# Kernel optimization log

Hardware: AMD Instinct MI355X
Metric: run time of the kernel (lower is better)

## Reference

```python
import jax, jax.numpy as jnp
import numpy as np

N = 50000      # nodes
E = 640000     # edges
DIN = 128      # input feature dim
DOUT = 128     # env net output dim
DACT = 2       # action net output dim (keep/drop logits)
REL = 100      # relation embedding dim (hard-coded in get_net)
T = 2          # num edge types
TAU = 0.5      # gumbel temperature (CoGNN temp)


def _lin(k, i, o):
    return jax.random.normal(k, (o, i), jnp.float32) * np.float32(1.0 / np.sqrt(i))


def _hgn_params(key, din, dout):
    ks = jax.random.split(key, 5)
    return {"W_w": _lin(ks[0], din, dout), "W_b": jnp.zeros((dout,), jnp.float32),
            "Wr_w": _lin(ks[1], REL, dout), "Wr_b": jnp.zeros((dout,), jnp.float32),
            "a_w": _lin(ks[2], 3 * dout, 1), "a_b": jnp.zeros((1,), jnp.float32),
            "Wres_w": _lin(ks[3], din, dout), "Wres_b": jnp.zeros((dout,), jnp.float32),
            "rel_emb": jax.random.normal(ks[4], (T, REL), jnp.float32)}


def setup_inputs():
    key = jax.random.key(0)
    ks = jax.random.split(key, 8)
    inp = {"x": jax.random.normal(ks[0], (N, DIN), jnp.float32),
           "edge_index": jax.random.randint(ks[1], (2, E), 0, N, jnp.int32),
           "edge_type": jax.random.randint(ks[2], (E,), 0, T, jnp.int32)}
    u_in = jax.random.uniform(ks[3], (N, DACT), jnp.float32, 1e-6, 1.0 - 1e-6)
    u_out = jax.random.uniform(ks[4], (N, DACT), jnp.float32, 1e-6, 1.0 - 1e-6)
    inp["g_in"] = -jnp.log(-jnp.log(u_in))    # Gumbel(0,1) noise
    inp["g_out"] = -jnp.log(-jnp.log(u_out))
    for name, k, dout in (("inA", ks[5], DACT), ("outA", ks[6], DACT), ("env", ks[7], DOUT)):
        for pk, pv in _hgn_params(k, DIN, dout).items():
            inp[name + "_" + pk] = pv
    return inp


def _simple_hgn(x, src, dst, etype, W_w, W_b, Wr_w, Wr_b, a_w, a_b, Wres_w, Wres_b, rel_emb, mask=None):
    # out = scatter_add_dst( alpha_e * W x_src ) + W_res x   (SimpleHGN, add aggr)
    n = x.shape[0]
    dout = W_w.shape[0]
    h = x @ W_w.T + W_b                       # [N, dout] = W(x)
    r = rel_emb @ Wr_w.T + Wr_b               # [T, dout] = W_r(rel_emb)
    # a(cat(W(x_i), W(x_j), W_r(rel))) decomposed into three per-node/per-type dot products
    a1, a2, a3 = a_w[0, :dout], a_w[0, dout:2 * dout], a_w[0, 2 * dout:]
    s_dst = h @ a1                            # [N]
    s_src = h @ a2                            # [N]
    s_rel = r @ a3                            # [T]
    logits = jax.nn.leaky_relu(s_dst[dst] + s_src[src] + s_rel[etype] + a_b[0], 0.2)  # [E]
    if mask is not None:
        logits = jnp.where(mask, logits, -1e9)
    m = jax.ops.segment_max(logits, dst, num_segments=n)
    e = jnp.exp(logits - m[dst])
    if mask is not None:
        e = jnp.where(mask, e, 0.0)
    denom = jax.ops.segment_sum(e, dst, num_segments=n)
    alpha = e / jnp.maximum(denom[dst], 1e-16)   # edge softmax over incoming edges of each target
    aggr = jax.ops.segment_sum(h[src] * alpha[:, None], dst, num_segments=n)
    return aggr + x @ Wres_w.T + Wres_b


def _gumbel_hard(logits, g):
    y = jax.nn.softmax((logits + g) / TAU, axis=-1)
    y_hard = jax.nn.one_hot(jnp.argmax(y, axis=-1), y.shape[-1], dtype=y.dtype)
    return y_hard + y - jax.lax.stop_gradient(y)   # straight-through (hard=True)


def reference(x, edge_index, edge_type, g_in, g_out,
              inA_W_w, inA_W_b, inA_Wr_w, inA_Wr_b, inA_a_w, inA_a_b, inA_Wres_w, inA_Wres_b, inA_rel_emb,
              outA_W_w, outA_W_b, outA_Wr_w, outA_Wr_b, outA_a_w, outA_a_b, outA_Wres_w, outA_Wres_b, outA_rel_emb,
              env_W_w, env_W_b, env_Wr_w, env_Wr_b, env_a_w, env_a_b, env_Wres_w, env_Wres_b, env_rel_emb):
    src, dst = edge_index[0], edge_index[1]
    in_logits = _simple_hgn(x, src, dst, edge_type, inA_W_w, inA_W_b, inA_Wr_w, inA_Wr_b,
                            inA_a_w, inA_a_b, inA_Wres_w, inA_Wres_b, inA_rel_emb)
    out_logits = _simple_hgn(x, src, dst, edge_type, outA_W_w, outA_W_b, outA_Wr_w, outA_Wr_b,
                             outA_a_w, outA_a_b, outA_Wres_w, outA_Wres_b, outA_rel_emb)
    in_p = _gumbel_hard(in_logits, g_in)
    out_p = _gumbel_hard(out_logits, g_out)
    edge_weight = in_p[:, 0][dst] * out_p[:, 0][src]   # keep_in[v] * keep_out[u]
    mask = edge_weight > 0                              # hard edge filtering, non-differentiable as in torch
    return _simple_hgn(x, src, dst, edge_type, env_W_w, env_W_b, env_Wr_w, env_Wr_b,
                       env_a_w, env_a_b, env_Wres_w, env_Wres_b, env_rel_emb, mask=mask)
```

## Files before the change

### kernel.cpp

```cpp
#include <hip/hip_runtime.h>
#include <hip/hip_bf16.h>
#include <hip/hip_fp16.h>
#include <cstddef>

#define N_NODES 50000
#define N_EDGES 640000
#define DEG_CAP 48

__device__ __forceinline__ float lrelu(float z) { return z >= 0.f ? z : 0.2f * z; }

__device__ __forceinline__ unsigned short f2bf(float f) {
    unsigned u = __builtin_bit_cast(unsigned, f);
    u += 0x7FFFu + ((u >> 16) & 1u);
    return (unsigned short)(u >> 16);
}
__device__ __forceinline__ float bf2f(unsigned short h) {
    unsigned u = ((unsigned)h) << 16;
    return __builtin_bit_cast(float, u);
}

typedef __attribute__((ext_vector_type(8))) short short8;
typedef __attribute__((ext_vector_type(4))) float floatx4;

__global__ __launch_bounds__(256) void k_setup(
    const float* __restrict__ x,
    const float* __restrict__ rel_in, const float* __restrict__ Wr_in,
    const float* __restrict__ Wrb_in,
    const float* __restrict__ rel_out, const float* __restrict__ Wr_out,
    const float* __restrict__ Wrb_out,
    const float* __restrict__ rel_env, const float* __restrict__ Wr_env,
    const float* __restrict__ Wrb_env,
    const float* __restrict__ Wi, const float* __restrict__ Wib,
    const float* __restrict__ WiR, const float* __restrict__ WiRb,
    const float* __restrict__ ai,
    const float* __restrict__ Wo, const float* __restrict__ Wob,
    const float* __restrict__ WoR, const float* __restrict__ WoRb,
    const float* __restrict__ ao,
    const float* __restrict__ eW, const float* __restrict__ eWb,
    const float* __restrict__ eWR, const float* __restrict__ ea,
    float* __restrict__ srel,
    unsigned short* __restrict__ wh, unsigned short* __restrict__ wl,
    float4* __restrict__ dstT, float4* __restrict__ srcPack,
    float4* __restrict__ res_pack, int* __restrict__ cursor)
{
    int b = blockIdx.x;
    int tid = threadIdx.x;

    if (b == 0) {
        __shared__ float red[256];
        __shared__ float rs[8];
        {
            int tt = tid >> 7, j = tid & 127;
            float acc = 0.f;
            for (int k = 0; k < 100; ++k) acc += rel_env[tt * 100 + k] * Wr_env[j * 100 + k];
            acc += Wrb_env[j];
            red[tid] = acc * ea[256 + j];
        }
        if (tid < 8) {
            int net = tid >> 2, tt = (tid >> 1) & 1, j = tid & 1;
            const float* re = net ? rel_out : rel_in;
            const float* wr = net ? Wr_out : Wr_in;
            const float* wb = net ? Wrb_out : Wrb_in;
            float acc = 0.f;
            for (int k = 0; k < 100; ++k) acc += re[tt * 100 + k] * wr[j * 100 + k];
            rs[tid] = acc + wb[j];
        }
        __syncthreads();
        if (tid < 2) {
            float s = 0.f;
            for (int j = 0; j < 128; ++j) s += red[tid * 128 + j];
            srel[4 + tid] = s;
        } else if (tid == 2) {
            srel[0] = rs[0] * ai[4] + rs[1] * ai[5];
            srel[1] = rs[2] * ai[4] + rs[3] * ai[5];
        } else if (tid == 3) {
            srel[2] = rs[4] * ao[4] + rs[5] * ao[5];
            srel[3] = rs[6] * ao[4] + rs[7] * ao[5];
        }
        return;
    }
    if (b < 129) {
        int i = (b - 1) * 256 + tid;
        float v = (i < 16384) ? eW[i] : eWR[i - 16384];
        unsigned short h = f2bf(v);
        wh[i] = h;
        wl[i] = f2bf(v - bf2f(h));
        return;
    }

    int n = (b - 129) * 256 + tid;
    if (n < N_NODES) cursor[n] = 0;

    __shared__ float sw[10][128];
    __shared__ float vb[2];
    {
        int row = tid >> 5, c4 = tid & 31;
        const float* src;
        switch (row) {
            case 0: src = Wi;        break;
            case 1: src = Wi + 128;  break;
            case 2: src = WiR;       break;
            case 3: src = WiR + 128; break;
            case 4: src = Wo;        break;
            case 5: src = Wo + 128;  break;
            case 6: src = WoR;       break;
            default: src = WoR + 128; break;
        }
        float4 v = ((const float4*)src)[c4];
        sw[row][c4 * 4 + 0] = v.x; sw[row][c4 * 4 + 1] = v.y;
        sw[row][c4 * 4 + 2] = v.z; sw[row][c4 * 4 + 3] = v.w;
    }
    {
        int half = tid >> 7, k = tid & 127;
        const float* av = ea + half * 128;
        float s = 0.f;
        for (int j = 0; j < 128; ++j) s += eW[j * 128 + k] * av[j];
        sw[8 + half][k] = s;
    }
    if (tid < 2) {
        const float* av2 = ea + tid * 128;
        float sb = 0.f;
        for (int j = 0; j < 128; ++j) sb += eWb[j] * av2[j];
        vb[tid] = sb;
    }
    __syncthreads();
    if (n >= N_NODES) return;
    const float4* xr = (const float4*)(x + (size_t)n * 128);
    float a0 = 0, a1 = 0, a2 = 0, a3 = 0, a4 = 0, a5 = 0, a6 = 0, a7 = 0;
    float a8 = 0, a9 = 0;
#pragma unroll 8
    for (int k4 = 0; k4 < 32; ++k4) {
        float4 v = xr[k4];
        int k = k4 * 4;
        a0 += v.x * sw[0][k] + v.y * sw[0][k + 1] + v.z * sw[0][k + 2] + v.w * sw[0][k + 3];
        a1 += v.x * sw[1][k] + v.y * sw[1][k + 1] + v.z * sw[1][k + 2] + v.w * sw[1][k + 3];
        a2 += v.x * sw[2][k] + v.y * sw[2][k + 1] + v.z * sw[2][k + 2] + v.w * sw[2][k + 3];
        a3 += v.x * sw[3][k] + v.y * sw[3][k + 1] + v.z * sw[3][k + 2] + v.w * sw[3][k + 3];
        a4 += v.x * sw[4][k] + v.y * sw[4][k + 1] + v.z * sw[4][k + 2] + v.w * sw[4][k + 3];
        a5 += v.x * sw[5][k] + v.y * sw[5][k + 1] + v.z * sw[5][k + 2] + v.w * sw[5][k + 3];
        a6 += v.x * sw[6][k] + v.y * sw[6][k + 1] + v.z * sw[6][k + 2] + v.w * sw[6][k + 3];
        a7 += v.x * sw[7][k] + v.y * sw[7][k + 1] + v.z * sw[7][k + 2] + v.w * sw[7][k + 3];
        a8 += v.x * sw[8][k] + v.y * sw[8][k + 1] + v.z * sw[8][k + 2] + v.w * sw[8][k + 3];
        a9 += v.x * sw[9][k] + v.y * sw[9][k + 1] + v.z * sw[9][k + 2] + v.w * sw[9][k + 3];
    }
    float hi0 = a0 + Wib[0], hi1 = a1 + Wib[1];
    float ri0 = a2 + WiRb[0], ri1 = a3 + WiRb[1];
    float ho0 = a4 + Wob[0], ho1 = a5 + Wob[1];
    float ro0 = a6 + WoRb[0], ro1 = a7 + WoRb[1];
    float sdi = hi0 * ai[0] + hi1 * ai[1];
    float ssi = hi0 * ai[2] + hi1 * ai[3];
    float sdo = ho0 * ao[0] + ho1 * ao[1];
    float sso = ho0 * ao[2] + ho1 * ao[3];
    dstT[n]           = make_float4(sdi, sdo, a8 + vb[0], 0.f);
    srcPack[2 * n]     = make_float4(ssi, sso, a9 + vb[1], 0.f);
    srcPack[2 * n + 1] = make_float4(hi0, hi1, ho0, ho1);
    res_pack[n]       = make_float4(ri0, ri1, ro0, ro1);
}

__global__ __launch_bounds__(256, 2) void k_mid(
    const float* __restrict__ x,
    const unsigned short* __restrict__ wh, const unsigned short* __restrict__ wl,
    const float* __restrict__ Wb, const float* __restrict__ WRb,
    __half* __restrict__ h_env, float* __restrict__ dout,
    const int* __restrict__ ei, const int* __restrict__ et,
    const float4* __restrict__ dstT, const float4* __restrict__ srcPack,
    const float* __restrict__ srel, const float* __restrict__ ab_env,
    int* __restrict__ cursor, unsigned long long* __restrict__ recs)
{
    int b = blockIdx.x;
    int tid = threadIdx.x;

    if (b >= 512) {
        int base = (b - 512) * 1024 + tid;
        float s4 = srel[4], s5 = srel[5];
        float abe = ab_env[0];
        int src[4], dst[4], t[4];
#pragma unroll
        for (int k = 0; k < 4; ++k) {
            int e = base + k * 256;
            src[k] = ei[e];
            dst[k] = ei[N_EDGES + e];
            t[k]   = et[e];
        }
        float4 dT[4], sT[4];
#pragma unroll
        for (int k = 0; k < 4; ++k) {
            dT[k] = dstT[dst[k]];
            sT[k] = srcPack[2 * src[k]];
        }
#pragma unroll
        for (int k = 0; k < 4; ++k) {
            float le = lrelu(dT[k].z + sT[k].z + (t[k] ? s5 : s4) + abe);
            int pos = atomicAdd(&cursor[dst[k]], 1);
            if (pos < DEG_CAP) {
                unsigned lo = (unsigned)(src[k] | (t[k] << 20));
                unsigned hi = (unsigned)__float_as_int(__expf(le));
                recs[dst[k] * DEG_CAP + pos] = ((unsigned long long)hi << 32) | lo;
            }
        }
        return;
    }

    int lane = tid & 63;
    int wv = tid >> 6;
    int l15 = lane & 15;
    int quad = lane >> 4;
    int jbase = wv * 64;

    short8 bh[4][4], bl[4][4];
    float bias[4];
#pragma unroll
    for (int jtl = 0; jtl < 4; ++jtl) {
        int j = jbase + jtl * 16 + l15;
        bias[jtl] = (j < 128) ? Wb[j] : WRb[j - 128];
#pragma unroll
        for (int ks = 0; ks < 4; ++ks) {
            size_t o = (size_t)j * 128 + ks * 32 + quad * 8;
            bh[jtl][ks] = *(const short8*)(wh + o);
            bl[jtl][ks] = *(const short8*)(wl + o);
        }
    }

    for (int t = b; t < 3125; t += 512) {
        int node = t * 16 + l15;
        const float4* ap = (const float4*)(x + (size_t)node * 128 + quad * 8);
        float4 f[8];
#pragma unroll
        for (int ks = 0; ks < 4; ++ks) {
            f[2 * ks]     = ap[ks * 8];
            f[2 * ks + 1] = ap[ks * 8 + 1];
        }
        short8 ah[4], al[4];
#pragma unroll
        for (int ks = 0; ks < 4; ++ks) {
            float av[8] = {f[2 * ks].x, f[2 * ks].y, f[2 * ks].z, f[2 * ks].w,
                           f[2 * ks + 1].x, f[2 * ks + 1].y, f[2 * ks + 1].z, f[2 * ks + 1].w};
#pragma unroll
            for (int i = 0; i < 8; ++i) {
                unsigned short h = f2bf(av[i]);
                ah[ks][i] = (short)h;
                al[ks][i] = (short)f2bf(av[i] - bf2f(h));
            }
        }
        floatx4 acc[4];
#pragma unroll
        for (int jtl = 0; jtl < 4; ++jtl) acc[jtl] = (floatx4)(0.f);
#pragma unroll
        for (int ks = 0; ks < 4; ++ks) {
#pragma unroll
            for (int jtl = 0; jtl < 4; ++jtl) {
                acc[jtl] = __builtin_amdgcn_mfma_f32_16x16x32_bf16(ah[ks], bh[jtl][ks], acc[jtl], 0, 0, 0);
                acc[jtl] = __builtin_amdgcn_mfma_f32_16x16x32_bf16(al[ks], bh[jtl][ks], acc[jtl], 0, 0, 0);
                acc[jtl] = __builtin_amdgcn_mfma_f32_16x16x32_bf16(ah[ks], bl[jtl][ks], acc[jtl], 0, 0, 0);
            }
        }
        int nb = t * 16 + quad * 4;
        if (wv < 2) {
#pragma unroll
            for (int jtl = 0; jtl < 4; ++jtl) {
                int j = jbase + jtl * 16 + l15;
#pragma unroll
                for (int r = 0; r < 4; ++r)
                    h_env[(size_t)(nb + r) * 128 + j] = __float2half(acc[jtl][r] + bias[jtl]);
            }
        } else {
#pragma unroll
            for (int jtl = 0; jtl < 4; ++jtl) {
                int j = jbase - 128 + jtl * 16 + l15;
#pragma unroll
                for (int r = 0; r < 4; ++r)
                    dout[(size_t)(nb + r) * 128 + j] = acc[jtl][r] + bias[jtl];
            }
        }
    }
}

__global__ __launch_bounds__(256) void k_action_seg(
    const int* __restrict__ cursor, const unsigned long long* __restrict__ recs,
    const float4* __restrict__ dstT, const float4* __restrict__ srcPack,
    const float4* __restrict__ res_pack,
    const float* __restrict__ srel,
    const float* __restrict__ ab_in, const float* __restrict__ ab_out,
    const float* __restrict__ g_in, const float* __restrict__ g_out,
    unsigned char* __restrict__ flags)
{
    int gid = blockIdx.x * 256 + threadIdx.x;
    int n = gid >> 2, sub = gid & 3;
    if (n >= N_NODES) return;
    int cnt = min(cursor[n], DEG_CAP);
    int st = n * DEG_CAP;
    float s0 = srel[0], s1 = srel[1], s2 = srel[2], s3 = srel[3];
    float abi = ab_in[0], abo = ab_out[0];
    float4 dT = dstT[n];
    float ni0 = 0, ni1 = 0, di = 0, no0 = 0, no1 = 0, dob = 0;
    for (int i = sub; i < cnt; i += 4) {
        unsigned long long rec = recs[st + i];
        int src = (int)(rec & 0xFFFFFu);
        int t = (int)((rec >> 20) & 0xFFFu);
        float4 sT = srcPack[2 * src];
        float4 hp = srcPack[2 * src + 1];
        float li = lrelu(dT.x + sT.x + (t ? s1 : s0) + abi);
        float lo = lrelu(dT.y + sT.y + (t ? s3 : s2) + abo);
        float ein = __expf(li), eout = __expf(lo);
        di  += ein;  ni0 += ein * hp.x;  ni1 += ein * hp.y;
        dob += eout; no0 += eout * hp.z; no1 += eout * hp.w;
    }
#pragma unroll
    for (int o = 1; o < 4; o <<= 1) {
        ni0 += __shfl_down(ni0, o); ni1 += __shfl_down(ni1, o);
        di  += __shfl_down(di,  o);
        no0 += __shfl_down(no0, o); no1 += __shfl_down(no1, o);
        dob += __shfl_down(dob, o);
    }
    if (sub == 0) {
        float4 rp = res_pack[n];
        float dinv = 1.f / fmaxf(di, 1e-16f);
        float l0 = ni0 * dinv + rp.x;
        float l1 = ni1 * dinv + rp.y;
        float2 gi = ((const float2*)g_in)[n];
        int in0 = (l0 + gi.x) >= (l1 + gi.y);
        float oinv = 1.f / fmaxf(dob, 1e-16f);
        float m0 = no0 * oinv + rp.z;
        float m1 = no1 * oinv + rp.w;
        float2 go = ((const float2*)g_out)[n];
        int out0 = (m0 + go.x) >= (m1 + go.y);
        flags[n] = (unsigned char)(in0 | (out0 << 1));
    }
}

__global__ __launch_bounds__(256) void k_aggr(
    const int* __restrict__ cursor,
    const unsigned long long* __restrict__ recs, const unsigned char* __restrict__ flags,
    const __half* __restrict__ h_env, float* __restrict__ dout)
{
    __shared__ int   s_src[4][64];
    __shared__ float s_w[4][64];
    int tid = threadIdx.x;
    int lane = tid & 63;
    int wv = tid >> 6;
    int n = blockIdx.x * 4 + wv;
    if (n >= N_NODES) return;
    if (!(flags[n] & 1)) return;
    int cnt = min(cursor[n], DEG_CAP);
    int st = n * DEG_CAP;
    float ax = 0.f, ay = 0.f, den = 0.f;
    const __half2* h2 = (const __half2*)h_env;
    {
        int i = lane;
        bool act = false; int src = 0; float wgt = 0.f;
        if (i < cnt) {
            unsigned long long rec = recs[st + i];
            src = (int)(rec & 0xFFFFFu);
            wgt = __int_as_float((int)(rec >> 32));
            act = (flags[src] & 2) != 0;
        }
        unsigned long long bal = __ballot(act);
        int m = __popcll(bal);
        if (act) {
            int pos = __popcll(bal & ((1ull << lane) - 1));
            s_src[wv][pos] = src;
            s_w[wv][pos] = wgt;
        }
        __builtin_amdgcn_wave_barrier();
        int k = 0;
        for (; k + 4 <= m; k += 4) {
            int s0 = s_src[wv][k], s1 = s_src[wv][k + 1];
            int s2 = s_src[wv][k + 2], s3 = s_src[wv][k + 3];
            float w0 = s_w[wv][k], w1 = s_w[wv][k + 1];
            float w2 = s_w[wv][k + 2], w3 = s_w[wv][k + 3];
            float2 f0 = __half22float2(h2[(size_t)s0 * 64 + lane]);
            float2 f1 = __half22float2(h2[(size_t)s1 * 64 + lane]);
            float2 f2 = __half22float2(h2[(size_t)s2 * 64 + lane]);
            float2 f3 = __half22float2(h2[(size_t)s3 * 64 + lane]);
            den += (w0 + w1) + (w2 + w3);
            ax += w0 * f0.x + w1 * f1.x + w2 * f2.x + w3 * f3.x;
            ay += w0 * f0.y + w1 * f1.y + w2 * f2.y + w3 * f3.y;
        }
        for (; k < m; ++k) {
            int s0 = s_src[wv][k];
            float w0 = s_w[wv][k];
            float2 f0 = __half22float2(h2[(size_t)s0 * 64 + lane]);
            den += w0; ax += w0 * f0.x; ay += w0 * f0.y;
        }
    }
    float inv = 1.f / fmaxf(den, 1e-16f);
    float2* op = (float2*)dout + (size_t)n * 64 + lane;
    float2 r = *op;
    r.x = ax * inv + r.x;
    r.y = ay * inv + r.y;
    *op = r;
}

extern "C" void kernel_launch(void* const* d_in, const int* in_sizes, int n_in,
                              void* d_out, int out_size, void* d_ws, size_t ws_size,
                              hipStream_t stream)
{
    const float* x     = (const float*)d_in[0];
    const int*   ei    = (const int*)d_in[1];
    const int*   et    = (const int*)d_in[2];
    const float* g_in  = (const float*)d_in[3];
    const float* g_out = (const float*)d_in[4];
    const float* iW   = (const float*)d_in[5];
    const float* iWb  = (const float*)d_in[6];
    const float* iWr  = (const float*)d_in[7];
    const float* iWrb = (const float*)d_in[8];
    const float* ia   = (const float*)d_in[9];
    const float* iab  = (const float*)d_in[10];
    const float* iWR  = (const float*)d_in[11];
    const float* iWRb = (const float*)d_in[12];
    const float* irel = (const float*)d_in[13];
    const float* oW   = (const float*)d_in[14];
    const float* oWb  = (const float*)d_in[15];
    const float* oWr  = (const float*)d_in[16];
    const float* oWrb = (const float*)d_in[17];
    const float* oa   = (const float*)d_in[18];
    const float* oab  = (const float*)d_in[19];
    const float* oWR  = (const float*)d_in[20];
    const float* oWRb = (const float*)d_in[21];
    const float* orel = (const float*)d_in[22];
    const float* eW   = (const float*)d_in[23];
    const float* eWb  = (const float*)d_in[24];
    const float* eWr  = (const float*)d_in[25];
    const float* eWrb = (const float*)d_in[26];
    const float* ea   = (const float*)d_in[27];
    const float* eab  = (const float*)d_in[28];
    const float* eWR  = (const float*)d_in[29];
    const float* eWRb = (const float*)d_in[30];
    const float* erel = (const float*)d_in[31];
    float* dout = (float*)d_out;

    char* w = (char*)d_ws;
    size_t off = 0;
    auto alloc = [&](size_t bytes) -> char* {
        char* p = w + off;
        off += (bytes + 255) & ~(size_t)255;
        return p;
    };
    int*   cursor  = (int*)alloc((size_t)N_NODES * 4);
    float* srel    = (float*)alloc(16 * 4);
    float4* dstT     = (float4*)alloc((size_t)4 * N_NODES * 4);
    float4* srcPack  = (float4*)alloc((size_t)8 * N_NODES * 4);
    float4* res_pack = (float4*)alloc((size_t)4 * N_NODES * 4);
    unsigned char* flags = (unsigned char*)alloc(N_NODES);
    unsigned short* wh = (unsigned short*)alloc((size_t)32768 * 2);
    unsigned short* wl = (unsigned short*)alloc((size_t)32768 * 2);
    unsigned long long* recs = (unsigned long long*)alloc((size_t)N_NODES * DEG_CAP * 8);
    __half* h_env    = (__half*)alloc((size_t)N_NODES * 128 * 2);

    k_setup<<<325, 256, 0, stream>>>(x,
                                     irel, iWr, iWrb, orel, oWr, oWrb, erel, eWr, eWrb,
                                     iW, iWb, iWR, iWRb, ia, oW, oWb, oWR, oWRb, oa,
                                     eW, eWb, eWR, ea,
                                     srel, wh, wl, dstT, srcPack, res_pack, cursor);
    k_mid<<<1137, 256, 0, stream>>>(x, wh, wl, eWb, eWRb, h_env, dout,
                                    ei, et, dstT, srcPack, srel, eab, cursor, recs);
    k_action_seg<<<782, 256, 0, stream>>>(cursor, recs, dstT, srcPack, res_pack,
                                          srel, iab, oab, g_in, g_out, flags);
    k_aggr<<<12500, 256, 0, stream>>>(cursor, recs, flags, h_env, dout);
}
```

Before: 233.7 us.

## Partition edge bucketing by destination range to localize atomics and record writes

The edge-bucketing blocks in k_mid are split into 8 destination-node ranges. Each block scans a 4096-edge chunk and only handles edges whose dst falls in its range, so each block's atomics and record writes land in a smaller, more cache-local region. The cost is that every edge's dst index is read 8 times and the grid grows to 1768 blocks. Separately, k_aggr now loads the dout value before the accumulation loop so that read latency overlaps with the gathers.

```diff
diff --git a/kernel.cpp b/kernel.cpp
--- a/kernel.cpp
+++ b/kernel.cpp
@@ -171,31 +171,28 @@
     int tid = threadIdx.x;
 
     if (b >= 512) {
-        int base = (b - 512) * 1024 + tid;
+        int bp = b - 512;
+        int j  = bp & 7;
+        int q  = bp >> 3;
+        int lo = j * 6250, hi = lo + 6250;
         float s4 = srel[4], s5 = srel[5];
         float abe = ab_env[0];
-        int src[4], dst[4], t[4];
-#pragma unroll
-        for (int k = 0; k < 4; ++k) {
-            int e = base + k * 256;
-            src[k] = ei[e];
-            dst[k] = ei[N_EDGES + e];
-            t[k]   = et[e];
-        }
-        float4 dT[4], sT[4];
-#pragma unroll
-        for (int k = 0; k < 4; ++k) {
-            dT[k] = dstT[dst[k]];
-            sT[k] = srcPack[2 * src[k]];
-        }
-#pragma unroll
-        for (int k = 0; k < 4; ++k) {
-            float le = lrelu(dT[k].z + sT[k].z + (t[k] ? s5 : s4) + abe);
-            int pos = atomicAdd(&cursor[dst[k]], 1);
+        int base = q * 4096;
+        for (int it = 0; it < 16; ++it) {
+            int e = base + it * 256 + tid;
+            if (e >= N_EDGES) break;
+            int dst = ei[N_EDGES + e];
+            if (dst < lo || dst >= hi) continue;
+            int src = ei[e];
+            int t = et[e];
+            float4 dT = dstT[dst];
+            float4 sT = srcPack[2 * src];
+            float le = lrelu(dT.z + sT.z + (t ? s5 : s4) + abe);
+            int pos = atomicAdd(&cursor[dst], 1);
             if (pos < DEG_CAP) {
-                unsigned lo = (unsigned)(src[k] | (t[k] << 20));
-                unsigned hi = (unsigned)__float_as_int(__expf(le));
-                recs[dst[k] * DEG_CAP + pos] = ((unsigned long long)hi << 32) | lo;
+                unsigned lov = (unsigned)(src | (t << 20));
+                unsigned hiv = (unsigned)__float_as_int(__expf(le));
+                recs[dst * DEG_CAP + pos] = ((unsigned long long)hiv << 32) | lov;
             }
         }
         return;
@@ -343,6 +340,8 @@
     if (!(flags[n] & 1)) return;
     int cnt = min(cursor[n], DEG_CAP);
     int st = n * DEG_CAP;
+    float2* op = (float2*)dout + (size_t)n * 64 + lane;
+    float2 r = *op;
     float ax = 0.f, ay = 0.f, den = 0.f;
     const __half2* h2 = (const __half2*)h_env;
     {
@@ -384,8 +383,6 @@
         }
     }
     float inv = 1.f / fmaxf(den, 1e-16f);
-    float2* op = (float2*)dout + (size_t)n * 64 + lane;
-    float2 r = *op;
     r.x = ax * inv + r.x;
     r.y = ay * inv + r.y;
     *op = r;
@@ -452,7 +449,7 @@
                                      iW, iWb, iWR, iWRb, ia, oW, oWb, oWR, oWRb, oa,
                                      eW, eWb, eWR, ea,
                                      srel, wh, wl, dstT, srcPack, res_pack, cursor);
-    k_mid<<<1137, 256, 0, stream>>>(x, wh, wl, eWb, eWRb, h_env, dout,
+    k_mid<<<1768, 256, 0, stream>>>(x, wh, wl, eWb, eWRb, h_env, dout,
                                     ei, et, dstT, srcPack, srel, eab, cursor, recs);
     k_action_seg<<<782, 256, 0, stream>>>(cursor, recs, dstT, srcPack, res_pack,
                                           srel, iab, oab, g_in, g_out, flags);
```

Result: slower. 283.6 us (+21.4%).
